# Kernel optimization log

Measured on AMD Instinct MI355X. Metric: run time of the kernel, lower is better.

Reference implementation:

```python
import jax, jax.numpy as jnp
import numpy as np

N = 50000
E = 1600000
IN_DIM = 128
HIDDEN = 128


def setup_inputs() -> dict:
    key = jax.random.key(0)
    ks = jax.random.split(key, 10)
    s = lambda d: 1.0 / np.sqrt(d)
    return {
        "x": jax.random.normal(ks[0], (N, IN_DIM), dtype=jnp.float32),
        "edge_index": jax.random.randint(ks[1], (2, E), 0, N, dtype=jnp.int64),
        "w1l": jax.random.normal(ks[2], (HIDDEN, IN_DIM), dtype=jnp.float32) * s(IN_DIM),
        "b1l": jnp.zeros((HIDDEN,), dtype=jnp.float32),
        "w1r": jax.random.normal(ks[3], (HIDDEN, IN_DIM), dtype=jnp.float32) * s(IN_DIM),
        "w2l": jax.random.normal(ks[4], (HIDDEN, HIDDEN), dtype=jnp.float32) * s(HIDDEN),
        "b2l": jnp.zeros((HIDDEN,), dtype=jnp.float32),
        "w2r": jax.random.normal(ks[5], (HIDDEN, HIDDEN), dtype=jnp.float32) * s(HIDDEN),
        "mw1": jax.random.normal(ks[6], (HIDDEN, HIDDEN), dtype=jnp.float32) * s(HIDDEN),
        "mb1": jnp.zeros((HIDDEN,), dtype=jnp.float32),
        "mw2": jax.random.normal(ks[7], (1, HIDDEN), dtype=jnp.float32) * s(HIDDEN),
        "mb2": jnp.zeros((1,), dtype=jnp.float32),
    }


def _mean_aggr(x, src, dst, num_nodes):
    # scatter-mean of source features onto target nodes (PyG SAGEConv mean aggr)
    summed = jax.ops.segment_sum(x[src], dst, num_segments=num_nodes)  # [N, D]
    count = jax.ops.segment_sum(jnp.ones((src.shape[0],), x.dtype), dst,
                                num_segments=num_nodes)
    return summed / jnp.maximum(count, 1.0)[:, None]


def _sage_conv(x, src, dst, wl, bl, wr):
    # out = lin_l(mean_aggr(x_neighbors)) + lin_r(x_root)
    aggr = _mean_aggr(x, src, dst, x.shape[0])
    return aggr @ wl.T + bl + x @ wr.T


def reference(x, edge_index, w1l, b1l, w1r, w2l, b2l, w2r, mw1, mb1, mw2, mb2):
    src, dst = edge_index[0], edge_index[1]
    h = jax.nn.relu(_sage_conv(x, src, dst, w1l, b1l, w1r))   # dropout: eval mode
    h = jax.nn.relu(_sage_conv(h, src, dst, w2l, b2l, w2r))
    h = jax.nn.relu(h @ mw1.T + mb1)
    logits = (h @ mw2.T + mb2).squeeze(-1)                    # [N]
    return logits
```

## Files before the change

### kernel.cpp

```cpp
#include <hip/hip_runtime.h>
#include <hip/hip_bf16.h>
#include <cstdint>

#define HD 128
#define BKSZ 256
#define BCAP 12288
#define EBIN 2048

typedef __attribute__((ext_vector_type(8))) short bfx8;
typedef __attribute__((ext_vector_type(4))) float fx4;

__device__ inline float bf2f(short s) {
    union { uint32_t u; float f; } c;
    c.u = ((uint32_t)(unsigned short)s) << 16;
    return c.f;
}
__device__ inline unsigned short f2bf(float v) {
    union { float f; uint32_t u; } c;
    c.f = v;
    uint32_t u = c.u + 0x7FFF + ((c.u >> 16) & 1);
    return (unsigned short)(u >> 16);
}

__device__ inline void stage_lds(const void* g, void* l, int nbytes) {
    const char* gc = (const char*)g;
    for (int off = threadIdx.x * 16; off < nbytes; off += 4096) {
        __builtin_amdgcn_global_load_lds(
            (const __attribute__((address_space(1))) unsigned int*)(gc + off),
            (__attribute__((address_space(3))) unsigned int*)
                ((__attribute__((address_space(3))) char*)l + off),
            16, 0, 0);
    }
}

__global__ void k_zero(int* __restrict__ p, int n) {
    for (int i = threadIdx.x; i < n; i += 256) p[i] = 0;
}


__global__ __launch_bounds__(256) void k_front(
    const int* __restrict__ ei, int E, int NBK,
    int* __restrict__ bcnt, int* __restrict__ bpack,
    const float* __restrict__ x, unsigned short* __restrict__ xb, int n8,
    const float* __restrict__ w0, const float* __restrict__ w1,
    const float* __restrict__ w2, const float* __restrict__ w3,
    const float* __restrict__ w4, unsigned short* __restrict__ wout,
    int nbin, int ncast) {
    __shared__ int lhist[BKSZ];
    __shared__ int gbase[BKSZ];

    int bid = blockIdx.x;
    if (bid < nbin) {
        int base = bid * EBIN;
        for (int i = threadIdx.x; i < NBK; i += 256) lhist[i] = 0;
        __syncthreads();

        int pw[8];
        int meta[8];
        const int4* s4 = (const int4*)ei;
        const int4* d4 = (const int4*)(ei + E);
        int c0 = base >> 2;
        int EC = E >> 2;
#pragma unroll
        for (int j = 0; j < 2; ++j) {
            int c4 = c0 + j * 256 + threadIdx.x;
            bool ok = (c4 < EC);
            int4 sv = make_int4(0, 0, 0, 0), dv = make_int4(0, 0, 0, 0);
            if (ok) { sv = s4[c4]; dv = d4[c4]; }
            int ss[4] = {sv.x, sv.y, sv.z, sv.w};
            int dd[4] = {dv.x, dv.y, dv.z, dv.w};
#pragma unroll
            for (int l = 0; l < 4; ++l) {
                int idx = j * 4 + l;
                meta[idx] = -1;
                if (ok) {
                    int d = dd[l];
                    int b = d >> 8;
                    int lr = atomicAdd(&lhist[b], 1);
                    pw[idx]   = ((d & 255) << 24) | ss[l];
                    meta[idx] = (b << 16) | lr;
                }
            }
        }
        __syncthreads();
        for (int i = threadIdx.x; i < NBK; i += 256) {
            int c = lhist[i];
            gbase[i] = c ? atomicAdd(&bcnt[i], c) : 0;
        }
        __syncthreads();
#pragma unroll
        for (int idx = 0; idx < 8; ++idx) {
            int m = meta[idx];
            if (m >= 0) {
                int b = m >> 16, lr = m & 0xFFFF;
                int pos = b * BCAP + min(gbase[b] + lr, BCAP - 1);
                bpack[pos] = pw[idx];
            }
        }
    } else if (bid < nbin + ncast) {
        int i = (bid - nbin) * 256 + threadIdx.x;
        if (i >= n8) return;
        float4 v0 = ((const float4*)x)[i * 2];
        float4 v1 = ((const float4*)x)[i * 2 + 1];
        bfx8 o;
        o[0] = (short)f2bf(v0.x); o[1] = (short)f2bf(v0.y);
        o[2] = (short)f2bf(v0.z); o[3] = (short)f2bf(v0.w);
        o[4] = (short)f2bf(v1.x); o[5] = (short)f2bf(v1.y);
        o[6] = (short)f2bf(v1.z); o[7] = (short)f2bf(v1.w);
        *(bfx8*)(xb + (size_t)i * 8) = o;
    } else {
        int t = (bid - nbin - ncast) * 256 + threadIdx.x;
        if (t >= 5 * 2048) return;
        int m = t / 2048, s = t % 2048;
        const float* src = (m == 0) ? w0 : (m == 1) ? w1 : (m == 2) ? w2
                                                   : (m == 3) ? w3 : w4;
        int l  = s & 63;
        int fi = s >> 6;
        int kk = fi >> 3;
        int cf = fi & 7;
        int r  = l & 15;
        int hi = l >> 4;
        int row  = cf * 16 + r;
        int col0 = kk * 32 + hi * 8;
        const float4* sp = (const float4*)(src + row * HD + col0);
        float4 v0 = sp[0];
        float4 v1 = sp[1];
        bfx8 o;
        o[0] = (short)f2bf(v0.x); o[1] = (short)f2bf(v0.y);
        o[2] = (short)f2bf(v0.z); o[3] = (short)f2bf(v0.w);
        o[4] = (short)f2bf(v1.x); o[5] = (short)f2bf(v1.y);
        o[6] = (short)f2bf(v1.z); o[7] = (short)f2bf(v1.w);
        *(bfx8*)(wout + (size_t)t * 8) = o;
    }
}

__global__ __launch_bounds__(512) void k_bucket(const int* __restrict__ bpack,
                                                const int* __restrict__ bcnt,
                                                int* __restrict__ offsets,
                                                int* __restrict__ sorted,
                                                int N, int E) {
    __shared__ int lh[BKSZ];
    __shared__ int cur[BKSZ];
    __shared__ int wsum[4];
    __shared__ int psum[8];
    int b = blockIdx.x;
    int tid = threadIdx.x;
    int lane = tid & 63;
    int wid = tid >> 6;

    int pv = (tid < b) ? bcnt[tid] : 0;
    int ps = pv;
#pragma unroll
    for (int s = 1; s < 64; s <<= 1) ps += __shfl_xor(ps, s, 64);
    if (lane == 0) psum[wid] = ps;

    int cnt = min(bcnt[b], BCAP);
    int base = b * BCAP;
    if (tid < BKSZ) lh[tid] = 0;
    __syncthreads();
    int obase = psum[0] + psum[1] + psum[2] + psum[3]
              + psum[4] + psum[5] + psum[6] + psum[7];

    for (int i = tid; i < cnt; i += 512)
        atomicAdd(&lh[((unsigned)bpack[base + i]) >> 24], 1);
    __syncthreads();

    if (tid < BKSZ) {
        int v = lh[tid];
        int sum = v;
#pragma unroll
        for (int s = 1; s < 64; s <<= 1) {
            int o = __shfl_up(sum, s, 64);
            if ((tid & 63) >= s) sum += o;
        }
        if ((tid & 63) == 63) wsum[wid] = sum;
        __syncthreads();
        int prefix = 0;
#pragma unroll
        for (int w = 0; w < 4; ++w)
            if (w < wid) prefix += wsum[w];
        int excl = prefix + sum - v;
        int n = b * BKSZ + tid;
        if (n < N) offsets[n] = obase + excl;
        cur[tid] = excl;
    } else {
        __syncthreads();
    }
    __syncthreads();

    for (int i = tid; i < cnt; i += 512) {
        int w = bpack[base + i];
        int ln = ((unsigned)w) >> 24;
        int p = atomicAdd(&cur[ln], 1);
        sorted[obase + p] = w & 0xFFFFFF;
    }
    if (b == 0 && tid == 0) offsets[N] = E;
}


__global__ __launch_bounds__(256) void k_aggr(const unsigned short* __restrict__ x,
                                              const int* __restrict__ offsets,
                                              const int* __restrict__ sorted_src,
                                              unsigned short* __restrict__ out, int N) {
    int wid  = threadIdx.x >> 6;
    int lane = threadIdx.x & 63;
    int n = blockIdx.x * 4 + wid;
    if (n >= N) return;
    int slot = lane >> 4;
    int c    = lane & 15;
    int beg = offsets[n], end = offsets[n + 1];

    float acc[8];
#pragma unroll
    for (int j = 0; j < 8; ++j) acc[j] = 0.f;

    int e = beg + slot;
    for (; e + 4 < end; e += 8) {
        int i0 = sorted_src[e];
        int i1 = sorted_src[e + 4];
        bfx8 v0 = *(const bfx8*)(x + (size_t)i0 * HD + c * 8);
        bfx8 v1 = *(const bfx8*)(x + (size_t)i1 * HD + c * 8);
#pragma unroll
        for (int j = 0; j < 8; ++j) acc[j] += bf2f(v0[j]);
#pragma unroll
        for (int j = 0; j < 8; ++j) acc[j] += bf2f(v1[j]);
    }
    if (e < end) {
        int i0 = sorted_src[e];
        bfx8 v0 = *(const bfx8*)(x + (size_t)i0 * HD + c * 8);
#pragma unroll
        for (int j = 0; j < 8; ++j) acc[j] += bf2f(v0[j]);
    }

#pragma unroll
    for (int j = 0; j < 8; ++j) {
        acc[j] += __shfl_xor(acc[j], 16, 64);
        acc[j] += __shfl_xor(acc[j], 32, 64);
    }
    if (slot == 0) {
        float inv = 1.f / fmaxf((float)(end - beg), 1.f);
        bfx8 o;
#pragma unroll
        for (int j = 0; j < 8; ++j) o[j] = (short)f2bf(acc[j] * inv);
        *(bfx8*)(out + (size_t)n * HD + c * 8) = o;
    }
}


__global__ __launch_bounds__(256) void k_gemm_mfma(
    const unsigned short* __restrict__ A,
    const unsigned short* __restrict__ B,
    const unsigned short* __restrict__ Wl,
    const unsigned short* __restrict__ Wr,
    const float* __restrict__ bias,
    unsigned short* __restrict__ outb, int nrows) {
    __shared__ bfx8 ldsW[4096];

    int wid  = threadIdx.x >> 6;
    int lane = threadIdx.x & 63;
    int r  = lane & 15;
    int hi = lane >> 4;
    int ko = hi * 8;
    int row0 = blockIdx.x * 64 + wid * 16;

    int arow  = row0 + r;
    int arowc = min(arow, nrows - 1);

    bfx8 a[4], b[4];
    const unsigned short* Ar = A + (size_t)arowc * HD;
    const unsigned short* Br = B + (size_t)arowc * HD;
#pragma unroll
    for (int kk = 0; kk < 4; ++kk) {
        a[kk] = *(const bfx8*)(Ar + kk * 32 + ko);
        b[kk] = *(const bfx8*)(Br + kk * 32 + ko);
    }

    stage_lds(Wl, &ldsW[0],    32768);
    stage_lds(Wr, &ldsW[2048], 32768);

    float bv[8];
#pragma unroll
    for (int cf = 0; cf < 8; ++cf) bv[cf] = bias[cf * 16 + r];

    fx4 acc[8];
#pragma unroll
    for (int cf = 0; cf < 8; ++cf) acc[cf] = (fx4){0.f, 0.f, 0.f, 0.f};

    __syncthreads();

#pragma unroll
    for (int kk = 0; kk < 4; ++kk) {
#pragma unroll
        for (int cf = 0; cf < 8; ++cf) {
            acc[cf] = __builtin_amdgcn_mfma_f32_16x16x32_bf16(
                a[kk], ldsW[(kk * 8 + cf) * 64 + lane], acc[cf], 0, 0, 0);
            acc[cf] = __builtin_amdgcn_mfma_f32_16x16x32_bf16(
                b[kk], ldsW[2048 + (kk * 8 + cf) * 64 + lane], acc[cf], 0, 0, 0);
        }
    }

#pragma unroll
    for (int cf = 0; cf < 8; ++cf) {
#pragma unroll
        for (int j = 0; j < 4; ++j) {
            int row = row0 + hi * 4 + j;
            if (row < nrows)
                outb[(size_t)row * HD + cf * 16 + r] = f2bf(fmaxf(acc[cf][j] + bv[cf], 0.f));
        }
    }
}


__global__ __launch_bounds__(256) void k_l2_fused(
    const unsigned short* __restrict__ A,
    const unsigned short* __restrict__ B,
    const unsigned short* __restrict__ Wl,
    const unsigned short* __restrict__ Wr,
    const float* __restrict__ bias,
    const unsigned short* __restrict__ Mw1,
    const float* __restrict__ mb1,
    const float* __restrict__ mw2,
    const float* __restrict__ mb2,
    float* __restrict__ outf, int nrows) {
    __shared__ bfx8 ldsW[4096];
    __shared__ unsigned short hlds[64 * HD];

    int wid  = threadIdx.x >> 6;
    int lane = threadIdx.x & 63;
    int r  = lane & 15;
    int hi = lane >> 4;
    int ko = hi * 8;
    int row0 = blockIdx.x * 64 + wid * 16;

    int arow  = row0 + r;
    int arowc = min(arow, nrows - 1);

    bfx8 a[4], b[4];
    const unsigned short* Ar = A + (size_t)arowc * HD;
    const unsigned short* Br = B + (size_t)arowc * HD;
#pragma unroll
    for (int kk = 0; kk < 4; ++kk) {
        a[kk] = *(const bfx8*)(Ar + kk * 32 + ko);
        b[kk] = *(const bfx8*)(Br + kk * 32 + ko);
    }

    stage_lds(Wl, &ldsW[0],    32768);
    stage_lds(Wr, &ldsW[2048], 32768);

    float bv[8];
#pragma unroll
    for (int cf = 0; cf < 8; ++cf) bv[cf] = bias[cf * 16 + r];

    fx4 acc[8];
#pragma unroll
    for (int cf = 0; cf < 8; ++cf) acc[cf] = (fx4){0.f, 0.f, 0.f, 0.f};

    __syncthreads();

#pragma unroll
    for (int kk = 0; kk < 4; ++kk) {
#pragma unroll
        for (int cf = 0; cf < 8; ++cf) {
            acc[cf] = __builtin_amdgcn_mfma_f32_16x16x32_bf16(
                a[kk], ldsW[(kk * 8 + cf) * 64 + lane], acc[cf], 0, 0, 0);
            acc[cf] = __builtin_amdgcn_mfma_f32_16x16x32_bf16(
                b[kk], ldsW[2048 + (kk * 8 + cf) * 64 + lane], acc[cf], 0, 0, 0);
        }
    }

#pragma unroll
    for (int cf = 0; cf < 8; ++cf) {
#pragma unroll
        for (int j = 0; j < 4; ++j) {
            int row_l = wid * 16 + hi * 4 + j;
            unsigned boff = (unsigned)(row_l * 256 + (cf * 16 + r) * 2);
            boff ^= (unsigned)((row_l & 7) << 4);
            *(unsigned short*)((char*)hlds + boff) = f2bf(fmaxf(acc[cf][j] + bv[cf], 0.f));
        }
    }
    __syncthreads();

    stage_lds(Mw1, &ldsW[0], 32768);

    bfx8 af[4];
    {
        int row_l = wid * 16 + r;
#pragma unroll
        for (int kk = 0; kk < 4; ++kk) {
            unsigned boff = (unsigned)(row_l * 256 + (kk * 32 + ko) * 2);
            boff ^= (unsigned)((row_l & 7) << 4);
            af[kk] = *(const bfx8*)((char*)hlds + boff);
        }
    }

    float m1v[8], m2v[8];
#pragma unroll
    for (int cf = 0; cf < 8; ++cf) {
        m1v[cf] = mb1[cf * 16 + r];
        m2v[cf] = mw2[cf * 16 + r];
    }

    fx4 acc2[8];
#pragma unroll
    for (int cf = 0; cf < 8; ++cf) acc2[cf] = (fx4){0.f, 0.f, 0.f, 0.f};

    __syncthreads();

#pragma unroll
    for (int kk = 0; kk < 4; ++kk) {
#pragma unroll
        for (int cf = 0; cf < 8; ++cf)
            acc2[cf] = __builtin_amdgcn_mfma_f32_16x16x32_bf16(
                af[kk], ldsW[(kk * 8 + cf) * 64 + lane], acc2[cf], 0, 0, 0);
    }

    float pd[4] = {0.f, 0.f, 0.f, 0.f};
#pragma unroll
    for (int cf = 0; cf < 8; ++cf) {
#pragma unroll
        for (int j = 0; j < 4; ++j)
            pd[j] += fmaxf(acc2[cf][j] + m1v[cf], 0.f) * m2v[cf];
    }

#pragma unroll
    for (int s = 1; s < 16; s <<= 1) {
#pragma unroll
        for (int j = 0; j < 4; ++j)
            pd[j] += __shfl_xor(pd[j], s, 64);
    }
    if (r == 0) {
        float mb = mb2[0];
#pragma unroll
        for (int j = 0; j < 4; ++j) {
            int row = row0 + hi * 4 + j;
            if (row < nrows) outf[row] = pd[j] + mb;
        }
    }
}


extern "C" void kernel_launch(void* const* d_in, const int* in_sizes, int n_in,
                              void* d_out, int out_size, void* d_ws, size_t ws_size,
                              hipStream_t stream) {
    const float* x   = (const float*)d_in[0];
    const int*   ei  = (const int*)d_in[1];
    const float* w1l = (const float*)d_in[2];
    const float* b1l = (const float*)d_in[3];
    const float* w1r = (const float*)d_in[4];
    const float* w2l = (const float*)d_in[5];
    const float* b2l = (const float*)d_in[6];
    const float* w2r = (const float*)d_in[7];
    const float* mw1 = (const float*)d_in[8];
    const float* mb1 = (const float*)d_in[9];
    const float* mw2 = (const float*)d_in[10];
    const float* mb2 = (const float*)d_in[11];
    float* out = (float*)d_out;

    const int N = in_sizes[0] / HD;
    const int E = in_sizes[1] / 2;
    const int NBK = (N + BKSZ - 1) / BKSZ;
    const int n8 = N * HD / 8;

    char* p = (char*)d_ws;
    auto alloc = [&](size_t bytes) -> char* {
        char* q = p;
        p += (bytes + 255) & ~(size_t)255;
        return q;
    };
    int*            bcnt    = (int*)alloc((size_t)NBK * 4);
    int*            offsets = (int*)alloc(((size_t)N + 1) * 4);
    int*            bpack   = (int*)alloc((size_t)NBK * BCAP * 4);
    int*            sorted  = (int*)alloc((size_t)E * 4);
    unsigned short* Wtb     = (unsigned short*)alloc((size_t)5 * HD * HD * 2);
    unsigned short* xb      = (unsigned short*)alloc((size_t)N * HD * 2);
    unsigned short* bufA    = (unsigned short*)alloc((size_t)N * HD * 2);
    unsigned short* bufB    = (unsigned short*)alloc((size_t)N * HD * 2);

    const unsigned short* W1l = Wtb + 0 * HD * HD;
    const unsigned short* W1r = Wtb + 1 * HD * HD;
    const unsigned short* W2l = Wtb + 2 * HD * HD;
    const unsigned short* W2r = Wtb + 3 * HD * HD;
    const unsigned short* Mw1 = Wtb + 4 * HD * HD;

    const int nbin  = (E + EBIN - 1) / EBIN;
    const int ncast = (n8 + 255) / 256;
    const int nc5   = 40;
    const int gb    = (N + 63) / 64;
    const int ab    = (N + 3) / 4;

    k_zero<<<1, 256, 0, stream>>>(bcnt, NBK);
    k_front<<<nbin + ncast + nc5, 256, 0, stream>>>(
        ei, E, NBK, bcnt, bpack, x, xb, n8,
        w1l, w1r, w2l, w2r, mw1, Wtb, nbin, ncast);
    k_bucket<<<NBK, 512, 0, stream>>>(bpack, bcnt, offsets, sorted, N, E);

    k_aggr<<<ab, 256, 0, stream>>>(xb, offsets, sorted, bufA, N);
    k_gemm_mfma<<<gb, 256, 0, stream>>>(bufA, xb, W1l, W1r, b1l, bufB, N);
    k_aggr<<<ab, 256, 0, stream>>>(bufB, offsets, sorted, bufA, N);
    k_l2_fused<<<gb, 256, 0, stream>>>(bufA, bufB, W2l, W2r, b2l, Mw1, mb1, mw2, mb2,
                                       out, N);
}
```

Before: 252.3 us.

## Replace capped bucket arrays with per-bin segments and bin×bucket count matrix

```diff
diff --git a/kernel.cpp b/kernel.cpp
--- a/kernel.cpp
+++ b/kernel.cpp
@@ -4,8 +4,7 @@
 
 #define HD 128
 #define BKSZ 256
-#define BCAP 12288
-#define EBIN 2048
+#define EBIN 1024
 
 typedef __attribute__((ext_vector_type(8))) short bfx8;
 typedef __attribute__((ext_vector_type(4))) float fx4;
@@ -40,61 +39,77 @@
 
 __global__ __launch_bounds__(256) void k_front(
     const int* __restrict__ ei, int E, int NBK,
-    int* __restrict__ bcnt, int* __restrict__ bpack,
+    int* __restrict__ bcnt, int* __restrict__ seg, int* __restrict__ mat,
     const float* __restrict__ x, unsigned short* __restrict__ xb, int n8,
     const float* __restrict__ w0, const float* __restrict__ w1,
     const float* __restrict__ w2, const float* __restrict__ w3,
     const float* __restrict__ w4, unsigned short* __restrict__ wout,
     int nbin, int ncast) {
     __shared__ int lhist[BKSZ];
-    __shared__ int gbase[BKSZ];
+    __shared__ int pstart[BKSZ];
+    __shared__ int wsum[4];
 
     int bid = blockIdx.x;
     if (bid < nbin) {
+        int tid = threadIdx.x;
         int base = bid * EBIN;
-        for (int i = threadIdx.x; i < NBK; i += 256) lhist[i] = 0;
+        lhist[tid] = 0;
         __syncthreads();
 
-        int pw[8];
-        int meta[8];
+        int pw[4];
+        int meta[4];
         const int4* s4 = (const int4*)ei;
         const int4* d4 = (const int4*)(ei + E);
-        int c0 = base >> 2;
+        int c4 = (base >> 2) + tid;
         int EC = E >> 2;
-#pragma unroll
-        for (int j = 0; j < 2; ++j) {
-            int c4 = c0 + j * 256 + threadIdx.x;
-            bool ok = (c4 < EC);
-            int4 sv = make_int4(0, 0, 0, 0), dv = make_int4(0, 0, 0, 0);
-            if (ok) { sv = s4[c4]; dv = d4[c4]; }
-            int ss[4] = {sv.x, sv.y, sv.z, sv.w};
-            int dd[4] = {dv.x, dv.y, dv.z, dv.w};
-#pragma unroll
-            for (int l = 0; l < 4; ++l) {
-                int idx = j * 4 + l;
-                meta[idx] = -1;
-                if (ok) {
-                    int d = dd[l];
-                    int b = d >> 8;
-                    int lr = atomicAdd(&lhist[b], 1);
-                    pw[idx]   = ((d & 255) << 24) | ss[l];
-                    meta[idx] = (b << 16) | lr;
-                }
+        bool ok = (c4 < EC);
+        int4 sv = make_int4(0, 0, 0, 0), dv = make_int4(0, 0, 0, 0);
+        if (ok) { sv = s4[c4]; dv = d4[c4]; }
+        int ss[4] = {sv.x, sv.y, sv.z, sv.w};
+        int dd[4] = {dv.x, dv.y, dv.z, dv.w};
+#pragma unroll
+        for (int l = 0; l < 4; ++l) {
+            meta[l] = -1;
+            if (ok) {
+                int d = dd[l];
+                int b = d >> 8;
+                int lr = atomicAdd(&lhist[b], 1);
+                pw[l]   = ((d & 255) << 24) | ss[l];
+                meta[l] = (b << 16) | lr;
             }
         }
         __syncthreads();
-        for (int i = threadIdx.x; i < NBK; i += 256) {
-            int c = lhist[i];
-            gbase[i] = c ? atomicAdd(&bcnt[i], c) : 0;
+
+        {
+            int lane = tid & 63, w = tid >> 6;
+            int v = lhist[tid];
+            int sum = v;
+#pragma unroll
+            for (int s = 1; s < 64; s <<= 1) {
+                int o = __shfl_up(sum, s, 64);
+                if (lane >= s) sum += o;
+            }
+            if (lane == 63) wsum[w] = sum;
+            __syncthreads();
+            int prefix = 0;
+#pragma unroll
+            for (int ww = 0; ww < 4; ++ww)
+                if (ww < w) prefix += wsum[ww];
+            pstart[tid] = prefix + sum - v;
+        }
+        if (tid < NBK) {
+            int c = lhist[tid];
+            mat[(size_t)bid * NBK + tid] = (pstart[tid] << 16) | c;
+            if (c) atomicAdd(&bcnt[tid], c);
         }
         __syncthreads();
-#pragma unroll
-        for (int idx = 0; idx < 8; ++idx) {
-            int m = meta[idx];
+
+#pragma unroll
+        for (int l = 0; l < 4; ++l) {
+            int m = meta[l];
             if (m >= 0) {
                 int b = m >> 16, lr = m & 0xFFFF;
-                int pos = b * BCAP + min(gbase[b] + lr, BCAP - 1);
-                bpack[pos] = pw[idx];
+                seg[base + pstart[b] + lr] = pw[l];
             }
         }
     } else if (bid < nbin + ncast) {
@@ -134,14 +149,16 @@
     }
 }
 
-__global__ __launch_bounds__(512) void k_bucket(const int* __restrict__ bpack,
+
+__global__ __launch_bounds__(512) void k_bucket(const int* __restrict__ seg,
+                                                const int* __restrict__ mat,
                                                 const int* __restrict__ bcnt,
                                                 int* __restrict__ offsets,
                                                 int* __restrict__ sorted,
-                                                int N, int E) {
+                                                int N, int E, int nbin, int NBK) {
     __shared__ int lh[BKSZ];
     __shared__ int cur[BKSZ];
-    __shared__ int wsum[4];
+    __shared__ int wsum[8];
     __shared__ int psum[8];
     int b = blockIdx.x;
     int tid = threadIdx.x;
@@ -154,57 +171,64 @@
     for (int s = 1; s < 64; s <<= 1) ps += __shfl_xor(ps, s, 64);
     if (lane == 0) psum[wid] = ps;
 
-    int cnt = min(bcnt[b], BCAP);
-    int base = b * BCAP;
     if (tid < BKSZ) lh[tid] = 0;
     __syncthreads();
     int obase = psum[0] + psum[1] + psum[2] + psum[3]
               + psum[4] + psum[5] + psum[6] + psum[7];
 
-    for (int i = tid; i < cnt; i += 512)
-        atomicAdd(&lh[((unsigned)bpack[base + i]) >> 24], 1);
-    __syncthreads();
-
-    if (tid < BKSZ) {
-        int v = lh[tid];
+    for (int s = tid; s < nbin; s += 512) {
+        int pc = mat[(size_t)s * NBK + b];
+        const int* sp = seg + s * EBIN + (pc >> 16);
+        int c = pc & 0xFFFF;
+        for (int j = 0; j < c; ++j)
+            atomicAdd(&lh[((unsigned)sp[j]) >> 24], 1);
+    }
+    __syncthreads();
+
+    {
+        int v = (tid < BKSZ) ? lh[tid] : 0;
         int sum = v;
 #pragma unroll
         for (int s = 1; s < 64; s <<= 1) {
             int o = __shfl_up(sum, s, 64);
-            if ((tid & 63) >= s) sum += o;
-        }
-        if ((tid & 63) == 63) wsum[wid] = sum;
+            if (lane >= s) sum += o;
+        }
+        if (lane == 63) wsum[wid] = sum;
         __syncthreads();
         int prefix = 0;
 #pragma unroll
         for (int w = 0; w < 4; ++w)
             if (w < wid) prefix += wsum[w];
-        int excl = prefix + sum - v;
-        int n = b * BKSZ + tid;
-        if (n < N) offsets[n] = obase + excl;
-        cur[tid] = excl;
-    } else {
-        __syncthreads();
-    }
-    __syncthreads();
-
-    for (int i = tid; i < cnt; i += 512) {
-        int w = bpack[base + i];
-        int ln = ((unsigned)w) >> 24;
-        int p = atomicAdd(&cur[ln], 1);
-        sorted[obase + p] = w & 0xFFFFFF;
+        if (tid < BKSZ) {
+            int excl = prefix + sum - v;
+            int n = b * BKSZ + tid;
+            if (n < N) offsets[n] = obase + excl;
+            cur[tid] = excl;
+        }
+    }
+    __syncthreads();
+
+    for (int s = tid; s < nbin; s += 512) {
+        int pc = mat[(size_t)s * NBK + b];
+        const int* sp = seg + s * EBIN + (pc >> 16);
+        int c = pc & 0xFFFF;
+        for (int j = 0; j < c; ++j) {
+            int w = sp[j];
+            int p = atomicAdd(&cur[((unsigned)w) >> 24], 1);
+            sorted[obase + p] = w & 0xFFFFFF;
+        }
     }
     if (b == 0 && tid == 0) offsets[N] = E;
 }
 
 
-__global__ __launch_bounds__(256) void k_aggr(const unsigned short* __restrict__ x,
-                                              const int* __restrict__ offsets,
-                                              const int* __restrict__ sorted_src,
-                                              unsigned short* __restrict__ out, int N) {
+__global__ __launch_bounds__(1024) void k_aggr(const unsigned short* __restrict__ x,
+                                               const int* __restrict__ offsets,
+                                               const int* __restrict__ sorted_src,
+                                               unsigned short* __restrict__ out, int N) {
     int wid  = threadIdx.x >> 6;
     int lane = threadIdx.x & 63;
-    int n = blockIdx.x * 4 + wid;
+    int n = blockIdx.x * 16 + wid;
     if (n >= N) return;
     int slot = lane >> 4;
     int c    = lane & 15;
@@ -461,6 +485,12 @@
     const int NBK = (N + BKSZ - 1) / BKSZ;
     const int n8 = N * HD / 8;
 
+    const int nbin  = (E + EBIN - 1) / EBIN;
+    const int ncast = (n8 + 255) / 256;
+    const int nc5   = 40;
+    const int gb    = (N + 63) / 64;
+    const int ab    = (N + 15) / 16;
+
     char* p = (char*)d_ws;
     auto alloc = [&](size_t bytes) -> char* {
         char* q = p;
@@ -469,7 +499,8 @@
     };
     int*            bcnt    = (int*)alloc((size_t)NBK * 4);
     int*            offsets = (int*)alloc(((size_t)N + 1) * 4);
-    int*            bpack   = (int*)alloc((size_t)NBK * BCAP * 4);
+    int*            seg     = (int*)alloc((size_t)nbin * EBIN * 4);
+    int*            mat     = (int*)alloc((size_t)nbin * NBK * 4);
     int*            sorted  = (int*)alloc((size_t)E * 4);
     unsigned short* Wtb     = (unsigned short*)alloc((size_t)5 * HD * HD * 2);
     unsigned short* xb      = (unsigned short*)alloc((size_t)N * HD * 2);
@@ -482,21 +513,15 @@
     const unsigned short* W2r = Wtb + 3 * HD * HD;
     const unsigned short* Mw1 = Wtb + 4 * HD * HD;
 
-    const int nbin  = (E + EBIN - 1) / EBIN;
-    const int ncast = (n8 + 255) / 256;
-    const int nc5   = 40;
-    const int gb    = (N + 63) / 64;
-    const int ab    = (N + 3) / 4;
-
     k_zero<<<1, 256, 0, stream>>>(bcnt, NBK);
     k_front<<<nbin + ncast + nc5, 256, 0, stream>>>(
-        ei, E, NBK, bcnt, bpack, x, xb, n8,
+        ei, E, NBK, bcnt, seg, mat, x, xb, n8,
         w1l, w1r, w2l, w2r, mw1, Wtb, nbin, ncast);
-    k_bucket<<<NBK, 512, 0, stream>>>(bpack, bcnt, offsets, sorted, N, E);
-
-    k_aggr<<<ab, 256, 0, stream>>>(xb, offsets, sorted, bufA, N);
+    k_bucket<<<NBK, 512, 0, stream>>>(seg, mat, bcnt, offsets, sorted, N, E, nbin, NBK);
+
+    k_aggr<<<ab, 1024, 0, stream>>>(xb, offsets, sorted, bufA, N);
     k_gemm_mfma<<<gb, 256, 0, stream>>>(bufA, xb, W1l, W1r, b1l, bufB, N);
-    k_aggr<<<ab, 256, 0, stream>>>(bufB, offsets, sorted, bufA, N);
+    k_aggr<<<ab, 1024, 0, stream>>>(bufB, offsets, sorted, bufA, N);
     k_l2_fused<<<gb, 256, 0, stream>>>(bufA, bufB, W2l, W2r, b2l, Mw1, mb1, mw2, mb2,
                                        out, N);
 }
```

Result: slower. 294.1 us (+16.5%).
